# Optimization experiments

Hardware: AMD Instinct MI355X
Metric: run time of the kernel (lower is better)

Reference implementation:

```python
import jax, jax.numpy as jnp
import numpy as np

B = 4096
FEATURE_SIZE = 64 * 64 * 10  # 40960 (HalfKP)
H1, H2, H3 = 256, 32, 32
NNZ = 30  # ~pieces on board per side


def _onehot_multi(key, batch, dim, nnz):
    # Build sparse feature vectors: nnz ones scattered per row (matches HalfKP usage).
    idx = jax.random.randint(key, (batch, nnz), 0, dim)
    x = jnp.zeros((batch, dim), dtype=jnp.float32)
    rows = jnp.arange(batch)[:, None]
    return x.at[rows, idx].set(1.0)


def setup_inputs() -> dict:
    key = jax.random.key(0)
    kw, kb, k1, k2, k3, k4, k5 = jax.random.split(key, 7)
    # xavier_uniform with gain=0.5: bound = 0.5 * sqrt(6/(fan_in+fan_out))
    def xavier(k, out_f, in_f):
        bound = 0.5 * np.sqrt(6.0 / (in_f + out_f))
        return jax.random.uniform(k, (out_f, in_f), jnp.float32, -bound, bound)
    return {
        "white_features": _onehot_multi(kw, B, FEATURE_SIZE, NNZ),
        "black_features": _onehot_multi(kb, B, FEATURE_SIZE, NNZ),
        "ft_w": xavier(k1, H1, FEATURE_SIZE),
        "ft_b": jnp.zeros((H1,), jnp.float32),
        "fc1_w": xavier(k2, H2, 2 * H1),
        "fc1_b": jnp.zeros((H2,), jnp.float32),
        "fc2_w": xavier(k3, H3, H2),
        "fc2_b": jnp.zeros((H3,), jnp.float32),
        "fc3_w": xavier(k4, 1, H3),
        "fc3_b": jnp.zeros((1,), jnp.float32),
    }


def _crelu(x):
    return jnp.clip(x, 0.0, 1.0)


def reference(white_features, black_features, ft_w, ft_b, fc1_w, fc1_b,
              fc2_w, fc2_b, fc3_w, fc3_b):
    # feature transform (dense equivalent of sparse gather-sum)
    w = _crelu(white_features @ ft_w.T + ft_b)  # [B, 256]
    b = _crelu(black_features @ ft_w.T + ft_b)  # [B, 256]
    x = jnp.concatenate([w, b], axis=1)          # [B, 512]
    x = _crelu(x @ fc1_w.T + fc1_b)              # [B, 32]
    x = _crelu(x @ fc2_w.T + fc2_b)              # [B, 32]
    return x @ fc3_w.T + fc3_b                   # [B, 1]
```

## Files before the change

kernel.cpp:

```cpp
#include <hip/hip_runtime.h>
#include <hip/hip_bf16.h>

#define FEAT 40960
#define NH1  256
#define MAXNZ 128

typedef float vfloat4 __attribute__((ext_vector_type(4)));

__global__ __launch_bounds__(256) void transpose_ftw(const float* __restrict__ ft_w,
                                                     float* __restrict__ ft_wt) {
    __shared__ float tile[32][33];
    const int i0 = blockIdx.x * 32;
    const int h0 = blockIdx.y * 32;
    const int tx = threadIdx.x;
    const int ty = threadIdx.y;
#pragma unroll
    for (int j = 0; j < 4; ++j) {
        tile[ty + j * 8][tx] = ft_w[(size_t)(h0 + ty + j * 8) * FEAT + i0 + tx];
    }
    __syncthreads();
#pragma unroll
    for (int j = 0; j < 4; ++j) {
        ft_wt[(size_t)(i0 + ty + j * 8) * NH1 + h0 + tx] = tile[tx][ty + j * 8];
    }
}

__global__ __launch_bounds__(256) void scan_compact(
    const float* __restrict__ wf,
    const float* __restrict__ bfeat,
    int B,
    int*   __restrict__ cnts,
    int*   __restrict__ lidx,
    float* __restrict__ lval)
{
    __shared__ int   idx[MAXNZ];
    __shared__ float val[MAXNZ];
    __shared__ int   cnt;

    const int tid = threadIdx.x;
    const int r   = blockIdx.x;
    const float* src = (r < B) ? (wf + (size_t)r * FEAT)
                               : (bfeat + (size_t)(r - B) * FEAT);
    if (tid == 0) cnt = 0;
    __syncthreads();

    const vfloat4* s4 = (const vfloat4*)src;
    constexpr int ITERS = FEAT / 4 / 256;
#pragma unroll 4
    for (int it = 0; it < ITERS; ++it) {
        const int k4 = it * 256 + tid;
        const vfloat4 v = __builtin_nontemporal_load(s4 + k4);
        const int base = k4 * 4;
        const bool any = (v.x != 0.f) | (v.y != 0.f) | (v.z != 0.f) | (v.w != 0.f);
        if (__any(any)) {
            if (v.x != 0.f) { int p = atomicAdd(&cnt, 1); if (p < MAXNZ) { idx[p] = base + 0; val[p] = v.x; } }
            if (v.y != 0.f) { int p = atomicAdd(&cnt, 1); if (p < MAXNZ) { idx[p] = base + 1; val[p] = v.y; } }
            if (v.z != 0.f) { int p = atomicAdd(&cnt, 1); if (p < MAXNZ) { idx[p] = base + 2; val[p] = v.z; } }
            if (v.w != 0.f) { int p = atomicAdd(&cnt, 1); if (p < MAXNZ) { idx[p] = base + 3; val[p] = v.w; } }
        }
    }
    __syncthreads();
    const int n = min(cnt, MAXNZ);
    if (tid == 0) cnts[r] = n;
    if (tid < n) {
        lidx[(size_t)r * MAXNZ + tid] = idx[tid];
        lval[(size_t)r * MAXNZ + tid] = val[tid];
    }
}

__global__ __launch_bounds__(256) void gather_mlp(
    const int*   __restrict__ cnts,
    const int*   __restrict__ lidx,
    const float* __restrict__ lval,
    int B,
    const float* __restrict__ ft_wt,
    const float* __restrict__ ft_b,
    const float* __restrict__ fc1_w,
    const float* __restrict__ fc1_b,
    const float* __restrict__ fc2_w,
    const float* __restrict__ fc2_b,
    const float* __restrict__ fc3_w,
    const float* __restrict__ fc3_b,
    float* __restrict__ out)
{
    __shared__ int   idxw[MAXNZ], idxb[MAXNZ];
    __shared__ float valw[MAXNZ], valb[MAXNZ];
    __shared__ float xsh[512];
    __shared__ float red[256];
    __shared__ float h1[32], h2[32];

    const int tid = threadIdx.x;
    const int b   = blockIdx.x;

    const int nw = cnts[b];
    const int nb = cnts[B + b];
    if (tid < nw) { idxw[tid] = lidx[(size_t)b * MAXNZ + tid];
                    valw[tid] = lval[(size_t)b * MAXNZ + tid]; }
    if (tid < nb) { idxb[tid] = lidx[(size_t)(B + b) * MAXNZ + tid];
                    valb[tid] = lval[(size_t)(B + b) * MAXNZ + tid]; }
    __syncthreads();

    float aw0 = ft_b[tid], aw1 = 0.f;
    float ab0 = aw0,       ab1 = 0.f;
    const int nmin = min(nw, nb);
    int j = 0;
    for (; j + 2 <= nmin; j += 2) {
        const float w0 = ft_wt[(size_t)idxw[j]     * NH1 + tid];
        const float w1 = ft_wt[(size_t)idxw[j + 1] * NH1 + tid];
        const float b0 = ft_wt[(size_t)idxb[j]     * NH1 + tid];
        const float b1 = ft_wt[(size_t)idxb[j + 1] * NH1 + tid];
        aw0 += valw[j] * w0;  aw1 += valw[j + 1] * w1;
        ab0 += valb[j] * b0;  ab1 += valb[j + 1] * b1;
    }
    for (int jw = j; jw < nw; ++jw) aw0 += valw[jw] * ft_wt[(size_t)idxw[jw] * NH1 + tid];
    for (int jb = j; jb < nb; ++jb) ab0 += valb[jb] * ft_wt[(size_t)idxb[jb] * NH1 + tid];

    xsh[tid]       = fminf(fmaxf(aw0 + aw1, 0.f), 1.f);
    xsh[256 + tid] = fminf(fmaxf(ab0 + ab1, 0.f), 1.f);
    __syncthreads();

    {
        const int o = tid & 31, part = tid >> 5;
        const float* wrow = fc1_w + o * 512 + part * 64;
        const float* xp   = xsh + part * 64;
        float s = 0.f;
#pragma unroll
        for (int k = 0; k < 64; ++k) s += wrow[k] * xp[k];
        red[tid] = s;
    }
    __syncthreads();
    if (tid < 32) {
        float s = fc1_b[tid];
#pragma unroll
        for (int p = 0; p < 8; ++p) s += red[tid + p * 32];
        h1[tid] = fminf(fmaxf(s, 0.f), 1.f);
    }
    __syncthreads();

    if (tid < 32) {
        float s = fc2_b[tid];
#pragma unroll
        for (int k = 0; k < 32; ++k) s += fc2_w[tid * 32 + k] * h1[k];
        h2[tid] = fminf(fmaxf(s, 0.f), 1.f);
    }
    __syncthreads();

    if (tid == 0) {
        float s = fc3_b[0];
#pragma unroll
        for (int k = 0; k < 32; ++k) s += fc3_w[k] * h2[k];
        out[b] = s;
    }
}

extern "C" void kernel_launch(void* const* d_in, const int* in_sizes, int n_in,
                              void* d_out, int out_size, void* d_ws, size_t ws_size,
                              hipStream_t stream) {
    const float* wf    = (const float*)d_in[0];
    const float* bfeat = (const float*)d_in[1];
    const float* ft_w  = (const float*)d_in[2];
    const float* ft_b  = (const float*)d_in[3];
    const float* fc1_w = (const float*)d_in[4];
    const float* fc1_b = (const float*)d_in[5];
    const float* fc2_w = (const float*)d_in[6];
    const float* fc2_b = (const float*)d_in[7];
    const float* fc3_w = (const float*)d_in[8];
    const float* fc3_b = (const float*)d_in[9];
    float* out = (float*)d_out;

    const int B = in_sizes[0] / FEAT;

    char* ws = (char*)d_ws;
    float* ft_wt = (float*)ws;
    int*   cnts  = (int*)  (ws + (48u << 20));
    int*   lidx  = (int*)  (ws + (52u << 20));
    float* lval  = (float*)(ws + (60u << 20));

    {
        dim3 blk(32, 8);
        dim3 grd(FEAT / 32, NH1 / 32);
        transpose_ftw<<<grd, blk, 0, stream>>>(ft_w, ft_wt);
    }
    scan_compact<<<2 * B, 256, 0, stream>>>(wf, bfeat, B, cnts, lidx, lval);
    gather_mlp<<<B, 256, 0, stream>>>(cnts, lidx, lval, B, ft_wt,
                                      ft_b, fc1_w, fc1_b, fc2_w, fc2_b,
                                      fc3_w, fc3_b, out);
}
```

Before: 1.261 ms.

## Replace per-row scan with flat grid-stride scan using global atomics

The per-row scan_compact kernel, which used shared-memory compaction and one block per row, is replaced by a flat grid-stride scan over the whole feature matrix. It uses 2048 blocks, unrolls 8 vector loads in flight per thread, and appends nonzeros with global atomics on per-row counters that are zeroed by a memset. The aim is to raise memory-level parallelism for the bandwidth-bound read of about 1.3 GB of dense one-hot input and to remove per-block sync overhead. The costs are an extra memset, global atomic contention, and a nondeterministic order of nonzeros within each row, which changes the float summation order.

Measured after the change: 1.320 ms. +4.7%, slower.

```diff
diff --git a/kernel.cpp b/kernel.cpp
--- a/kernel.cpp
+++ b/kernel.cpp
@@ -5,7 +5,8 @@
 #define NH1  256
 #define MAXNZ 128
 
-typedef float vfloat4 __attribute__((ext_vector_type(4)));
+typedef float        vfloat4 __attribute__((ext_vector_type(4)));
+typedef unsigned int vuint4  __attribute__((ext_vector_type(4)));
 
 __global__ __launch_bounds__(256) void transpose_ftw(const float* __restrict__ ft_w,
                                                      float* __restrict__ ft_wt) {
@@ -25,7 +26,7 @@
     }
 }
 
-__global__ __launch_bounds__(256) void scan_compact(
+__global__ __launch_bounds__(256) void scan_flat(
     const float* __restrict__ wf,
     const float* __restrict__ bfeat,
     int B,
@@ -33,38 +34,57 @@
     int*   __restrict__ lidx,
     float* __restrict__ lval)
 {
-    __shared__ int   idx[MAXNZ];
-    __shared__ float val[MAXNZ];
-    __shared__ int   cnt;
-
-    const int tid = threadIdx.x;
-    const int r   = blockIdx.x;
-    const float* src = (r < B) ? (wf + (size_t)r * FEAT)
-                               : (bfeat + (size_t)(r - B) * FEAT);
-    if (tid == 0) cnt = 0;
-    __syncthreads();
-
-    const vfloat4* s4 = (const vfloat4*)src;
-    constexpr int ITERS = FEAT / 4 / 256;
-#pragma unroll 4
-    for (int it = 0; it < ITERS; ++it) {
-        const int k4 = it * 256 + tid;
-        const vfloat4 v = __builtin_nontemporal_load(s4 + k4);
-        const int base = k4 * 4;
-        const bool any = (v.x != 0.f) | (v.y != 0.f) | (v.z != 0.f) | (v.w != 0.f);
-        if (__any(any)) {
-            if (v.x != 0.f) { int p = atomicAdd(&cnt, 1); if (p < MAXNZ) { idx[p] = base + 0; val[p] = v.x; } }
-            if (v.y != 0.f) { int p = atomicAdd(&cnt, 1); if (p < MAXNZ) { idx[p] = base + 1; val[p] = v.y; } }
-            if (v.z != 0.f) { int p = atomicAdd(&cnt, 1); if (p < MAXNZ) { idx[p] = base + 2; val[p] = v.z; } }
-            if (v.w != 0.f) { int p = atomicAdd(&cnt, 1); if (p < MAXNZ) { idx[p] = base + 3; val[p] = v.w; } }
+    const int  half    = gridDim.x >> 1;
+    const bool black   = (blockIdx.x >= half);
+    const int  sideBlk = black ? (blockIdx.x - half) : blockIdx.x;
+    const vuint4* s4   = (const vuint4*)(black ? bfeat : wf);
+    const int  rbase   = black ? B : 0;
+    const int  tpg     = half * 256;
+    const int  t0      = sideBlk * 256 + (int)threadIdx.x;
+    const int  total4  = (B >> 2) * FEAT;
+    const int  q4      = FEAT / 4;
+
+    constexpr int U = 8;
+    const int ng = total4 / (tpg * U);
+
+    for (int g = 0; g < ng; ++g) {
+        vuint4 v[U];
+        int    e[U];
+#pragma unroll
+        for (int u = 0; u < U; ++u) {
+            e[u] = (g * U + u) * tpg + t0;
+            v[u] = __builtin_nontemporal_load(s4 + e[u]);
         }
-    }
-    __syncthreads();
-    const int n = min(cnt, MAXNZ);
-    if (tid == 0) cnts[r] = n;
-    if (tid < n) {
-        lidx[(size_t)r * MAXNZ + tid] = idx[tid];
-        lval[(size_t)r * MAXNZ + tid] = val[tid];
+#pragma unroll
+        for (int u = 0; u < U; ++u) {
+            const unsigned x = v[u].x, y = v[u].y, z = v[u].z, w = v[u].w;
+            if (__any((x | y | z | w) != 0u)) {
+                const int row  = e[u] / q4;
+                const int base = (e[u] - row * q4) * 4;
+                const int r    = rbase + row;
+                int*   cp = cnts + r;
+                size_t lb = (size_t)r * MAXNZ;
+                if (x) { int p = atomicAdd(cp, 1); if (p < MAXNZ) { lidx[lb + p] = base + 0; lval[lb + p] = __uint_as_float(x); } }
+                if (y) { int p = atomicAdd(cp, 1); if (p < MAXNZ) { lidx[lb + p] = base + 1; lval[lb + p] = __uint_as_float(y); } }
+                if (z) { int p = atomicAdd(cp, 1); if (p < MAXNZ) { lidx[lb + p] = base + 2; lval[lb + p] = __uint_as_float(z); } }
+                if (w) { int p = atomicAdd(cp, 1); if (p < MAXNZ) { lidx[lb + p] = base + 3; lval[lb + p] = __uint_as_float(w); } }
+            }
+        }
+    }
+    for (int e4 = ng * (tpg * U) + t0; e4 < total4; e4 += tpg) {
+        const vuint4 v = __builtin_nontemporal_load(s4 + e4);
+        const unsigned x = v.x, y = v.y, z = v.z, w = v.w;
+        if (__any((x | y | z | w) != 0u)) {
+            const int row  = e4 / q4;
+            const int base = (e4 - row * q4) * 4;
+            const int r    = rbase + row;
+            int*   cp = cnts + r;
+            size_t lb = (size_t)r * MAXNZ;
+            if (x) { int p = atomicAdd(cp, 1); if (p < MAXNZ) { lidx[lb + p] = base + 0; lval[lb + p] = __uint_as_float(x); } }
+            if (y) { int p = atomicAdd(cp, 1); if (p < MAXNZ) { lidx[lb + p] = base + 1; lval[lb + p] = __uint_as_float(y); } }
+            if (z) { int p = atomicAdd(cp, 1); if (p < MAXNZ) { lidx[lb + p] = base + 2; lval[lb + p] = __uint_as_float(z); } }
+            if (w) { int p = atomicAdd(cp, 1); if (p < MAXNZ) { lidx[lb + p] = base + 3; lval[lb + p] = __uint_as_float(w); } }
+        }
     }
 }
 
@@ -92,8 +112,8 @@
     const int tid = threadIdx.x;
     const int b   = blockIdx.x;
 
-    const int nw = cnts[b];
-    const int nb = cnts[B + b];
+    const int nw = min(cnts[b], MAXNZ);
+    const int nb = min(cnts[B + b], MAXNZ);
     if (tid < nw) { idxw[tid] = lidx[(size_t)b * MAXNZ + tid];
                     valw[tid] = lval[(size_t)b * MAXNZ + tid]; }
     if (tid < nb) { idxb[tid] = lidx[(size_t)(B + b) * MAXNZ + tid];
@@ -176,12 +196,14 @@
     int*   lidx  = (int*)  (ws + (52u << 20));
     float* lval  = (float*)(ws + (60u << 20));
 
+    hipMemsetAsync(cnts, 0, (size_t)2 * B * sizeof(int), stream);
+
     {
         dim3 blk(32, 8);
         dim3 grd(FEAT / 32, NH1 / 32);
         transpose_ftw<<<grd, blk, 0, stream>>>(ft_w, ft_wt);
     }
-    scan_compact<<<2 * B, 256, 0, stream>>>(wf, bfeat, B, cnts, lidx, lval);
+    scan_flat<<<2048, 256, 0, stream>>>(wf, bfeat, B, cnts, lidx, lval);
     gather_mlp<<<B, 256, 0, stream>>>(cnts, lidx, lval, B, ft_wt,
                                       ft_b, fc1_w, fc1_b, fc2_w, fc2_b,
                                       fc3_w, fc3_b, out);
```
